# Kernel tuning notes

Hardware: AMD Instinct MI355X
Metric: run time of the kernel (lower is better)

Reference implementation:

```python
import jax, jax.numpy as jnp
import numpy as np

W_IMG = 512
H_IMG = 512
D_MODEL = 192
N_FREQ = 8
LN_EPS = 1e-5


def _fourier_pe(coords_norm):
    # coords_norm: [B,K,2] in [0,1); returns [B,K,4*N_FREQ]
    freqs = 2.0 ** jnp.arange(N_FREQ, dtype=jnp.float32)  # [F]
    two_pi = 2.0 * jnp.pi
    x = coords_norm[..., 0:1] * freqs * two_pi  # [B,K,F]
    y = coords_norm[..., 1:2] * freqs * two_pi
    return jnp.concatenate([jnp.sin(x), jnp.cos(x), jnp.sin(y), jnp.cos(y)], axis=-1)


def _bilinear_sample(feat, gx, gy):
    # feat: [B,C,H,W]; gx,gy: [B,K] normalized coords in [-1,1], align_corners=True
    B, C, H, W = feat.shape
    ix = (gx + 1.0) * 0.5 * (W - 1)
    iy = (gy + 1.0) * 0.5 * (H - 1)
    ix0 = jnp.floor(ix)
    iy0 = jnp.floor(iy)
    wx = ix - ix0  # [B,K]
    wy = iy - iy0
    x0 = jnp.clip(ix0.astype(jnp.int32), 0, W - 1)
    x1 = jnp.clip(ix0.astype(jnp.int32) + 1, 0, W - 1)
    y0 = jnp.clip(iy0.astype(jnp.int32), 0, H - 1)
    y1 = jnp.clip(iy0.astype(jnp.int32) + 1, 0, H - 1)
    b = jnp.arange(B)[:, None]  # [B,1] broadcast against [B,K]
    g = lambda y, x: feat[b, :, y, x]  # [B,K,C]
    out = (g(y0, x0) * ((1 - wx) * (1 - wy))[..., None]
           + g(y0, x1) * (wx * (1 - wy))[..., None]
           + g(y1, x0) * ((1 - wx) * wy)[..., None]
           + g(y1, x1) * (wx * wy)[..., None])
    return out  # [B,K,C]


def setup_inputs() -> dict:
    key = jax.random.key(0)
    ks = jax.random.split(key, 16)
    B, K = 8, 4096
    # pixel coordinates in [0, W_IMG-1] x [0, H_IMG-1]
    u = jax.random.uniform(ks[0], (B, K, 2), dtype=jnp.float32)
    coords = u * jnp.array([W_IMG - 1, H_IMG - 1], dtype=jnp.float32)
    L1 = jax.random.normal(ks[1], (B, D_MODEL, 128, 128), dtype=jnp.float32)
    L2 = jax.random.normal(ks[2], (B, D_MODEL, 64, 64), dtype=jnp.float32)
    L3 = jax.random.normal(ks[3], (B, D_MODEL, 32, 32), dtype=jnp.float32)
    L4 = jax.random.normal(ks[4], (B, D_MODEL, 16, 16), dtype=jnp.float32)
    d_in = D_MODEL * 4 + 4 * N_FREQ  # 800
    Wseed_w = jax.random.normal(ks[5], (D_MODEL, d_in), dtype=jnp.float32) / np.sqrt(d_in)
    Wseed_b = jnp.zeros((D_MODEL,), dtype=jnp.float32)
    ln_g = jnp.ones((D_MODEL,), dtype=jnp.float32)
    ln_b = jnp.zeros((D_MODEL,), dtype=jnp.float32)
    Wpos_w = jax.random.normal(ks[6], (D_MODEL, 4 * N_FREQ), dtype=jnp.float32) / np.sqrt(4 * N_FREQ)
    Wpos_b = jnp.zeros((D_MODEL,), dtype=jnp.float32)
    return {"coords": coords, "L1": L1, "L2": L2, "L3": L3, "L4": L4,
            "Wseed_w": Wseed_w, "Wseed_b": Wseed_b, "ln_g": ln_g, "ln_b": ln_b,
            "Wpos_w": Wpos_w, "Wpos_b": Wpos_b}


def reference(coords, L1, L2, L3, L4, Wseed_w, Wseed_b, ln_g, ln_b, Wpos_w, Wpos_b):
    B, K, _ = coords.shape
    # normalized grid in [-1,1] (x uses W, y uses H), align_corners=True convention
    gx = 2.0 * coords[..., 0] / (W_IMG - 1) - 1.0  # [B,K]
    gy = 2.0 * coords[..., 1] / (H_IMG - 1) - 1.0
    center_grid = jnp.stack([gx, gy], axis=-1).reshape(B, K, 1, 2)
    coords_norm = coords / jnp.array([W_IMG, H_IMG], dtype=jnp.float32)
    pe_q = _fourier_pe(coords_norm)  # [B,K,32]
    f1 = _bilinear_sample(L1, gx, gy)
    f2 = _bilinear_sample(L2, gx, gy)
    f3 = _bilinear_sample(L3, gx, gy)
    f4 = _bilinear_sample(L4, gx, gy)
    x = jnp.concatenate([f1, f2, f3, f4, pe_q], axis=-1)  # [B,K,800]
    seed = x @ Wseed_w.T + Wseed_b
    mu = jnp.mean(seed, axis=-1, keepdims=True)
    var = jnp.mean((seed - mu) ** 2, axis=-1, keepdims=True)
    seed = (seed - mu) / jnp.sqrt(var + LN_EPS) * ln_g + ln_b
    pos = pe_q @ Wpos_w.T + Wpos_b
    return (seed, pos, center_grid)
```

## Files before the change

kernel.cpp:

```cpp
#include <hip/hip_runtime.h>
#include <hip/hip_bf16.h>
#include <stdint.h>

typedef unsigned short u16;
typedef short s16x8 __attribute__((ext_vector_type(8)));
typedef float f32x4 __attribute__((ext_vector_type(4)));
typedef uint32_t u32x4 __attribute__((ext_vector_type(4)));

__device__ __forceinline__ uint32_t pack_bf16(float lo, float hi) {
  float2 f; f.x = lo; f.y = hi;
  __hip_bfloat162 h = __float22bfloat162_rn(f);
  union { __hip_bfloat162 h; uint32_t u; } c; c.h = h;
  return c.u;
}
__device__ __forceinline__ u16 f2bf(float f) {
  union { float f; uint32_t u; } a; a.f = f;
  uint32_t u = a.u;
  return (u16)((u + 0x7fffu + ((u >> 16) & 1u)) >> 16);
}
__device__ __forceinline__ float bf2f(uint32_t hbits) {
  union { uint32_t u; float f; } a; a.u = hbits << 16;
  return a.f;
}

__global__ __launch_bounds__(256) void prep_all(
    const float* __restrict__ L1, const float* __restrict__ L2,
    const float* __restrict__ L3, const float* __restrict__ L4,
    const float* __restrict__ ws_w, const float* __restrict__ wp_w,
    u16* __restrict__ T1, u16* __restrict__ T2,
    u16* __restrict__ T3, u16* __restrict__ T4,
    u16* __restrict__ dWs, u16* __restrict__ dWp) {
  const int bid = blockIdx.x;
  const int t = threadIdx.x;

  if (bid >= 2720) {
    int t0 = (bid - 2720) * 256 + t;
    for (int i = t0; i < 39936; i += 8192) {
      const float* s; u16* d; int off;
      if (i < 38400) { s = ws_w; d = dWs; off = 4 * i; }
      else           { s = wp_w; d = dWp; off = 4 * (i - 38400); }
      f32x4 v = *(const f32x4*)(s + off);
      uint2 o;
      o.x = pack_bf16(v.x, v.y);
      o.y = pack_bf16(v.z, v.w);
      *(uint2*)(d + off) = o;
    }
    return;
  }

  const float* src; u16* dst; int HW, tiles, rel;
  if (bid < 2048)      { src = L1; dst = T1; HW = 16384; tiles = 256; rel = bid; }
  else if (bid < 2560) { src = L2; dst = T2; HW = 4096;  tiles = 64;  rel = bid - 2048; }
  else if (bid < 2688) { src = L3; dst = T3; HW = 1024;  tiles = 16;  rel = bid - 2560; }
  else                 { src = L4; dst = T4; HW = 256;   tiles = 4;   rel = bid - 2688; }
  const int b = rel / tiles, hw0 = (rel % tiles) * 64;

  __shared__ uint32_t tileD[96 * 65];
  const float* sb = src + (size_t)b * 192 * HW + hw0;
  for (int i = 0; i < 6; ++i) {
    int idx = i * 256 + t;
    int c2 = idx >> 4, hw4 = idx & 15;
    f32x4 a = *(const f32x4*)(sb + (size_t)(2 * c2) * HW + hw4 * 4);
    f32x4 c = *(const f32x4*)(sb + (size_t)(2 * c2 + 1) * HW + hw4 * 4);
    uint32_t* w = &tileD[c2 * 65 + hw4 * 4];
    w[0] = pack_bf16(a.x, c.x);
    w[1] = pack_bf16(a.y, c.y);
    w[2] = pack_bf16(a.z, c.z);
    w[3] = pack_bf16(a.w, c.w);
  }
  __syncthreads();
  uint32_t* d = (uint32_t*)(dst + ((size_t)b * HW + hw0) * 192);
  for (int i = 0; i < 12; ++i) {
    int e = i * 256 + t;
    int hw = e / 48, cp = e - hw * 48;
    uint2 v;
    v.x = tileD[(cp * 2) * 65 + hw];
    v.y = tileD[(cp * 2 + 1) * 65 + hw];
    *(uint2*)(d + hw * 96 + cp * 2) = v;
  }
}

__global__ __launch_bounds__(256, 4) void seed_main(
    const float* __restrict__ coords,
    const u16* __restrict__ T1, const u16* __restrict__ T2,
    const u16* __restrict__ T3, const u16* __restrict__ T4,
    const u16* __restrict__ Wseed, const u16* __restrict__ Wpos,
    const float* __restrict__ seed_b, const float* __restrict__ ln_g,
    const float* __restrict__ ln_b, const float* __restrict__ pos_b,
    float* __restrict__ out_seed, float* __restrict__ out_pos,
    float* __restrict__ out_cg) {

  __shared__ __align__(16) u16 xt[16 * 808];
  __shared__ float mu_s[16], rs_s[16];

  const int t = threadIdx.x;
  const int gp0 = blockIdx.x * 16;
  const int b = gp0 >> 12;

  if (t < 32) {
    int p = t >> 1, xy = t & 1;
    float c = coords[(gp0 + p) * 2 + xy];
    out_cg[(gp0 + p) * 2 + xy] = c * (2.0f / 511.0f) - 1.0f;
  }
  for (int i = 0; i < 2; ++i) {
    int e = i * 256 + t;
    int p = e >> 5, j = e & 31;
    float c = coords[(gp0 + p) * 2 + ((j >> 4) & 1)] * (1.0f / 512.0f);
    float v = c * (float)(1 << (j & 7));
    float a = (v - floorf(v)) * 6.283185307179586f;
    float r = (j & 8) ? __cosf(a) : __sinf(a);
    xt[p * 808 + 768 + j] = f2bf(r);
  }

  {
    const u16* B1 = T1 + (size_t)b * 16384 * 192;
    const u16* B2 = T2 + (size_t)b * 4096 * 192;
    const u16* B3 = T3 + (size_t)b * 1024 * 192;
    const u16* B4 = T4 + (size_t)b * 256 * 192;
    int plv = t >> 2;
    int lv = plv & 3, p = plv >> 2;
    int c4b = t & 3;
    float cx = coords[(gp0 + p) * 2 + 0];
    float cy = coords[(gp0 + p) * 2 + 1];
    float gx = cx * (2.0f / 511.0f) - 1.0f;
    float gy = cy * (2.0f / 511.0f) - 1.0f;
    int Wl = 128 >> lv;
    float ix = (gx + 1.0f) * 0.5f * (float)(Wl - 1);
    float iy = (gy + 1.0f) * 0.5f * (float)(Wl - 1);
    float fx = floorf(ix), fy = floorf(iy);
    float wx = ix - fx, wy = iy - fy;
    int x0 = (int)fx, y0 = (int)fy;
    int x1 = min(max(x0 + 1, 0), Wl - 1), y1 = min(max(y0 + 1, 0), Wl - 1);
    x0 = min(max(x0, 0), Wl - 1); y0 = min(max(y0, 0), Wl - 1);
    const u16* base = (lv == 0) ? B1 : (lv == 1) ? B2 : (lv == 2) ? B3 : B4;
    const u16* b00 = base + (y0 * Wl + x0) * 192;
    const u16* b01 = base + (y0 * Wl + x1) * 192;
    const u16* b10 = base + (y1 * Wl + x0) * 192;
    const u16* b11 = base + (y1 * Wl + x1) * 192;
    float w00 = (1.0f - wx) * (1.0f - wy), w01 = wx * (1.0f - wy);
    float w10 = (1.0f - wx) * wy,          w11 = wx * wy;
    u16* dstp = xt + p * 808 + lv * 192;
#pragma unroll
    for (int i = 0; i < 6; ++i) {
      int cc = (c4b + 4 * i) * 8;
      u32x4 q00 = *(const u32x4*)(b00 + cc);
      u32x4 q01 = *(const u32x4*)(b01 + cc);
      u32x4 q10 = *(const u32x4*)(b10 + cc);
      u32x4 q11 = *(const u32x4*)(b11 + cc);
      u32x4 o;
#pragma unroll
      for (int k = 0; k < 4; ++k) {
        float lo = bf2f(q00[k] & 0xffff) * w00 + bf2f(q01[k] & 0xffff) * w01 +
                   bf2f(q10[k] & 0xffff) * w10 + bf2f(q11[k] & 0xffff) * w11;
        float hi = bf2f(q00[k] >> 16) * w00 + bf2f(q01[k] >> 16) * w01 +
                   bf2f(q10[k] >> 16) * w10 + bf2f(q11[k] >> 16) * w11;
        o[k] = pack_bf16(lo, hi);
      }
      *(u32x4*)(dstp + cc) = o;
    }
  }
  __syncthreads();

  const int lid = t & 63, wv = t >> 6;
  const int quad = lid >> 4, mrow = lid & 15;
  const int nt0 = wv * 3;

  f32x4 accS[3], accP[3];
#pragma unroll
  for (int j = 0; j < 3; ++j) { accS[j] = (f32x4)0.0f; accP[j] = (f32x4)0.0f; }

  const u16* wp0 = Wseed + (size_t)((nt0 + 0) * 16 + mrow) * 800 + quad * 8;
  const u16* wp1 = wp0 + 16 * 800;
  const u16* wp2 = wp1 + 16 * 800;
  const u16* arow = xt + mrow * 808 + quad * 8;

  s16x8 a_last;
#pragma unroll 5
  for (int kc = 0; kc < 25; ++kc) {
    int ko = kc * 32;
    s16x8 a = *(const s16x8*)(arow + ko);
    s16x8 b0 = *(const s16x8*)(wp0 + ko);
    s16x8 b1 = *(const s16x8*)(wp1 + ko);
    s16x8 b2 = *(const s16x8*)(wp2 + ko);
    accS[0] = __builtin_amdgcn_mfma_f32_16x16x32_bf16(a, b0, accS[0], 0, 0, 0);
    accS[1] = __builtin_amdgcn_mfma_f32_16x16x32_bf16(a, b1, accS[1], 0, 0, 0);
    accS[2] = __builtin_amdgcn_mfma_f32_16x16x32_bf16(a, b2, accS[2], 0, 0, 0);
    if (kc == 24) a_last = a;
  }
#pragma unroll
  for (int j = 0; j < 3; ++j) {
    int n = (nt0 + j) * 16 + mrow;
    s16x8 bw = *(const s16x8*)(Wpos + n * 32 + quad * 8);
    accP[j] = __builtin_amdgcn_mfma_f32_16x16x32_bf16(a_last, bw, accP[j], 0, 0, 0);
  }

#pragma unroll
  for (int j = 0; j < 3; ++j) {
    int n = (nt0 + j) * 16 + mrow;
    float pb = pos_b[n];
#pragma unroll
    for (int r = 0; r < 4; ++r)
      out_pos[(size_t)(gp0 + quad * 4 + r) * 192 + n] = accP[j][r] + pb;
  }

  __syncthreads();
  float* preLN = (float*)xt;
#pragma unroll
  for (int j = 0; j < 3; ++j) {
    int n = (nt0 + j) * 16 + mrow;
    float sb = seed_b[n];
#pragma unroll
    for (int r = 0; r < 4; ++r)
      preLN[(quad * 4 + r) * 193 + n] = accS[j][r] + sb;
  }
  __syncthreads();

  {
    int r = t >> 4, g = t & 15;
    float s = 0.0f, sq = 0.0f;
#pragma unroll
    for (int i = 0; i < 12; ++i) {
      float v = preLN[r * 193 + g * 12 + i];
      s += v; sq += v * v;
    }
#pragma unroll
    for (int d = 8; d > 0; d >>= 1) {
      s += __shfl_down(s, d, 16);
      sq += __shfl_down(sq, d, 16);
    }
    if (g == 0) {
      float mu = s * (1.0f / 192.0f);
      float var = sq * (1.0f / 192.0f) - mu * mu;
      mu_s[r] = mu;
      rs_s[r] = 1.0f / sqrtf(var + 1e-5f);
    }
  }
  __syncthreads();

  for (int i = 0; i < 12; ++i) {
    int e = i * 256 + t;
    int r = e / 192, n = e - r * 192;
    float v = (preLN[r * 193 + n] - mu_s[r]) * rs_s[r] * ln_g[n] + ln_b[n];
    out_seed[(size_t)(gp0 + r) * 192 + n] = v;
  }
}

extern "C" void kernel_launch(void* const* d_in, const int* in_sizes, int n_in,
                              void* d_out, int out_size, void* d_ws, size_t ws_size,
                              hipStream_t stream) {
  const float* coords  = (const float*)d_in[0];
  const float* L1      = (const float*)d_in[1];
  const float* L2      = (const float*)d_in[2];
  const float* L3      = (const float*)d_in[3];
  const float* L4      = (const float*)d_in[4];
  const float* Wseed_w = (const float*)d_in[5];
  const float* Wseed_b = (const float*)d_in[6];
  const float* ln_g    = (const float*)d_in[7];
  const float* ln_b    = (const float*)d_in[8];
  const float* Wpos_w  = (const float*)d_in[9];
  const float* Wpos_b  = (const float*)d_in[10];

  u16* T1  = (u16*)d_ws;
  u16* T2  = T1 + (size_t)8 * 16384 * 192;
  u16* T3  = T2 + (size_t)8 * 4096 * 192;
  u16* T4  = T3 + (size_t)8 * 1024 * 192;
  u16* Wsd = T4 + (size_t)8 * 256 * 192;
  u16* Wps = Wsd + 153600;

  prep_all<<<2752, 256, 0, stream>>>(L1, L2, L3, L4, Wseed_w, Wpos_w,
                                     T1, T2, T3, T4, Wsd, Wps);

  float* out_seed = (float*)d_out;
  float* out_pos  = out_seed + (size_t)32768 * 192;
  float* out_cg   = out_pos  + (size_t)32768 * 192;

  seed_main<<<2048, 256, 0, stream>>>(coords, T1, T2, T3, T4, Wsd, Wps,
                                      Wseed_b, ln_g, ln_b, Wpos_b,
                                      out_seed, out_pos, out_cg);
}
```

Measured before the change: 273.9 us.

## Process 32 points per block, prefetch GEMM operands, fuse LayerNorm in registers

Result: slower. 279.5 us (+2.0%).

```diff
diff --git a/kernel.cpp b/kernel.cpp
--- a/kernel.cpp
+++ b/kernel.cpp
@@ -80,7 +80,7 @@
   }
 }
 
-__global__ __launch_bounds__(256, 4) void seed_main(
+__global__ __launch_bounds__(256, 3) void seed_main(
     const float* __restrict__ coords,
     const u16* __restrict__ T1, const u16* __restrict__ T2,
     const u16* __restrict__ T3, const u16* __restrict__ T4,
@@ -90,19 +90,19 @@
     float* __restrict__ out_seed, float* __restrict__ out_pos,
     float* __restrict__ out_cg) {
 
-  __shared__ __align__(16) u16 xt[16 * 808];
-  __shared__ float mu_s[16], rs_s[16];
+  __shared__ __align__(16) u16 xt[32 * 808];
+  __shared__ float part_s[32][4], part_q[32][4];
 
   const int t = threadIdx.x;
-  const int gp0 = blockIdx.x * 16;
+  const int gp0 = blockIdx.x * 32;
   const int b = gp0 >> 12;
 
-  if (t < 32) {
+  if (t < 64) {
     int p = t >> 1, xy = t & 1;
     float c = coords[(gp0 + p) * 2 + xy];
     out_cg[(gp0 + p) * 2 + xy] = c * (2.0f / 511.0f) - 1.0f;
   }
-  for (int i = 0; i < 2; ++i) {
+  for (int i = 0; i < 4; ++i) {
     int e = i * 256 + t;
     int p = e >> 5, j = e & 31;
     float c = coords[(gp0 + p) * 2 + ((j >> 4) & 1)] * (1.0f / 512.0f);
@@ -117,9 +117,9 @@
     const u16* B2 = T2 + (size_t)b * 4096 * 192;
     const u16* B3 = T3 + (size_t)b * 1024 * 192;
     const u16* B4 = T4 + (size_t)b * 256 * 192;
-    int plv = t >> 2;
+    int plv = t >> 1;
     int lv = plv & 3, p = plv >> 2;
-    int c4b = t & 3;
+    int half = t & 1;
     float cx = coords[(gp0 + p) * 2 + 0];
     float cy = coords[(gp0 + p) * 2 + 1];
     float gx = cx * (2.0f / 511.0f) - 1.0f;
@@ -133,30 +133,36 @@
     int x1 = min(max(x0 + 1, 0), Wl - 1), y1 = min(max(y0 + 1, 0), Wl - 1);
     x0 = min(max(x0, 0), Wl - 1); y0 = min(max(y0, 0), Wl - 1);
     const u16* base = (lv == 0) ? B1 : (lv == 1) ? B2 : (lv == 2) ? B3 : B4;
-    const u16* b00 = base + (y0 * Wl + x0) * 192;
-    const u16* b01 = base + (y0 * Wl + x1) * 192;
-    const u16* b10 = base + (y1 * Wl + x0) * 192;
-    const u16* b11 = base + (y1 * Wl + x1) * 192;
+    const u16* b00 = base + (y0 * Wl + x0) * 192 + half * 96;
+    const u16* b01 = base + (y0 * Wl + x1) * 192 + half * 96;
+    const u16* b10 = base + (y1 * Wl + x0) * 192 + half * 96;
+    const u16* b11 = base + (y1 * Wl + x1) * 192 + half * 96;
     float w00 = (1.0f - wx) * (1.0f - wy), w01 = wx * (1.0f - wy);
     float w10 = (1.0f - wx) * wy,          w11 = wx * wy;
-    u16* dstp = xt + p * 808 + lv * 192;
-#pragma unroll
-    for (int i = 0; i < 6; ++i) {
-      int cc = (c4b + 4 * i) * 8;
-      u32x4 q00 = *(const u32x4*)(b00 + cc);
-      u32x4 q01 = *(const u32x4*)(b01 + cc);
-      u32x4 q10 = *(const u32x4*)(b10 + cc);
-      u32x4 q11 = *(const u32x4*)(b11 + cc);
-      u32x4 o;
+    u16* dstp = xt + p * 808 + lv * 192 + half * 96;
+#pragma unroll
+    for (int ii = 0; ii < 6; ++ii) {
+      int ca = ii * 16, cb = ii * 16 + 8;
+      u32x4 qa00 = *(const u32x4*)(b00 + ca), qb00 = *(const u32x4*)(b00 + cb);
+      u32x4 qa01 = *(const u32x4*)(b01 + ca), qb01 = *(const u32x4*)(b01 + cb);
+      u32x4 qa10 = *(const u32x4*)(b10 + ca), qb10 = *(const u32x4*)(b10 + cb);
+      u32x4 qa11 = *(const u32x4*)(b11 + ca), qb11 = *(const u32x4*)(b11 + cb);
+      u32x4 oa, ob;
 #pragma unroll
       for (int k = 0; k < 4; ++k) {
-        float lo = bf2f(q00[k] & 0xffff) * w00 + bf2f(q01[k] & 0xffff) * w01 +
-                   bf2f(q10[k] & 0xffff) * w10 + bf2f(q11[k] & 0xffff) * w11;
-        float hi = bf2f(q00[k] >> 16) * w00 + bf2f(q01[k] >> 16) * w01 +
-                   bf2f(q10[k] >> 16) * w10 + bf2f(q11[k] >> 16) * w11;
-        o[k] = pack_bf16(lo, hi);
-      }
-      *(u32x4*)(dstp + cc) = o;
+        float lo = bf2f(qa00[k] & 0xffff) * w00 + bf2f(qa01[k] & 0xffff) * w01 +
+                   bf2f(qa10[k] & 0xffff) * w10 + bf2f(qa11[k] & 0xffff) * w11;
+        float hi = bf2f(qa00[k] >> 16) * w00 + bf2f(qa01[k] >> 16) * w01 +
+                   bf2f(qa10[k] >> 16) * w10 + bf2f(qa11[k] >> 16) * w11;
+        oa[k] = pack_bf16(lo, hi);
+        lo = bf2f(qb00[k] & 0xffff) * w00 + bf2f(qb01[k] & 0xffff) * w01 +
+             bf2f(qb10[k] & 0xffff) * w10 + bf2f(qb11[k] & 0xffff) * w11;
+        hi = bf2f(qb00[k] >> 16) * w00 + bf2f(qb01[k] >> 16) * w01 +
+             bf2f(qb10[k] >> 16) * w10 + bf2f(qb11[k] >> 16) * w11;
+        ob[k] = pack_bf16(lo, hi);
+      }
+      *(u32x4*)(dstp + ca) = oa;
+      *(u32x4*)(dstp + cb) = ob;
     }
   }
   __syncthreads();
@@ -165,83 +171,120 @@
   const int quad = lid >> 4, mrow = lid & 15;
   const int nt0 = wv * 3;
 
-  f32x4 accS[3], accP[3];
-#pragma unroll
-  for (int j = 0; j < 3; ++j) { accS[j] = (f32x4)0.0f; accP[j] = (f32x4)0.0f; }
-
-  const u16* wp0 = Wseed + (size_t)((nt0 + 0) * 16 + mrow) * 800 + quad * 8;
-  const u16* wp1 = wp0 + 16 * 800;
-  const u16* wp2 = wp1 + 16 * 800;
-  const u16* arow = xt + mrow * 808 + quad * 8;
-
-  s16x8 a_last;
-#pragma unroll 5
+  const u16* arow0 = xt + mrow * 808 + quad * 8;
+  const u16* arow1 = arow0 + 16 * 808;
+  const u16* w0 = Wseed + (size_t)((nt0 + 0) * 16 + mrow) * 800 + quad * 8;
+  const u16* w1 = w0 + 16 * 800;
+  const u16* w2 = w1 + 16 * 800;
+
+  f32x4 accS[2][3];
+#pragma unroll
+  for (int mt = 0; mt < 2; ++mt)
+#pragma unroll
+    for (int j = 0; j < 3; ++j) accS[mt][j] = (f32x4)0.0f;
+
+  s16x8 abuf[3][2], bbuf[3][3];
+#pragma unroll
+  for (int s = 0; s < 3; ++s) {
+    int ko = s * 32;
+    abuf[s][0] = *(const s16x8*)(arow0 + ko);
+    abuf[s][1] = *(const s16x8*)(arow1 + ko);
+    bbuf[s][0] = *(const s16x8*)(w0 + ko);
+    bbuf[s][1] = *(const s16x8*)(w1 + ko);
+    bbuf[s][2] = *(const s16x8*)(w2 + ko);
+  }
+#pragma unroll
   for (int kc = 0; kc < 25; ++kc) {
-    int ko = kc * 32;
-    s16x8 a = *(const s16x8*)(arow + ko);
-    s16x8 b0 = *(const s16x8*)(wp0 + ko);
-    s16x8 b1 = *(const s16x8*)(wp1 + ko);
-    s16x8 b2 = *(const s16x8*)(wp2 + ko);
-    accS[0] = __builtin_amdgcn_mfma_f32_16x16x32_bf16(a, b0, accS[0], 0, 0, 0);
-    accS[1] = __builtin_amdgcn_mfma_f32_16x16x32_bf16(a, b1, accS[1], 0, 0, 0);
-    accS[2] = __builtin_amdgcn_mfma_f32_16x16x32_bf16(a, b2, accS[2], 0, 0, 0);
-    if (kc == 24) a_last = a;
-  }
+    const int cur = kc % 3;
+    s16x8 a0 = abuf[cur][0], a1 = abuf[cur][1];
+    s16x8 b0 = bbuf[cur][0], b1 = bbuf[cur][1], b2 = bbuf[cur][2];
+    int nk = kc + 3;
+    if (nk < 25) {
+      int ko = nk * 32;
+      abuf[cur][0] = *(const s16x8*)(arow0 + ko);
+      abuf[cur][1] = *(const s16x8*)(arow1 + ko);
+      bbuf[cur][0] = *(const s16x8*)(w0 + ko);
+      bbuf[cur][1] = *(const s16x8*)(w1 + ko);
+      bbuf[cur][2] = *(const s16x8*)(w2 + ko);
+    }
+    accS[0][0] = __builtin_amdgcn_mfma_f32_16x16x32_bf16(a0, b0, accS[0][0], 0, 0, 0);
+    accS[1][0] = __builtin_amdgcn_mfma_f32_16x16x32_bf16(a1, b0, accS[1][0], 0, 0, 0);
+    accS[0][1] = __builtin_amdgcn_mfma_f32_16x16x32_bf16(a0, b1, accS[0][1], 0, 0, 0);
+    accS[1][1] = __builtin_amdgcn_mfma_f32_16x16x32_bf16(a1, b1, accS[1][1], 0, 0, 0);
+    accS[0][2] = __builtin_amdgcn_mfma_f32_16x16x32_bf16(a0, b2, accS[0][2], 0, 0, 0);
+    accS[1][2] = __builtin_amdgcn_mfma_f32_16x16x32_bf16(a1, b2, accS[1][2], 0, 0, 0);
+  }
+
+  {
+    s16x8 ap0 = *(const s16x8*)(arow0 + 768);
+    s16x8 ap1 = *(const s16x8*)(arow1 + 768);
+#pragma unroll
+    for (int j = 0; j < 3; ++j) {
+      int n = (nt0 + j) * 16 + mrow;
+      s16x8 bw = *(const s16x8*)(Wpos + n * 32 + quad * 8);
+      f32x4 p0 = (f32x4)0.0f, p1 = (f32x4)0.0f;
+      p0 = __builtin_amdgcn_mfma_f32_16x16x32_bf16(ap0, bw, p0, 0, 0, 0);
+      p1 = __builtin_amdgcn_mfma_f32_16x16x32_bf16(ap1, bw, p1, 0, 0, 0);
+      float pb = pos_b[n];
+#pragma unroll
+      for (int r = 0; r < 4; ++r) {
+        out_pos[(size_t)(gp0 + quad * 4 + r) * 192 + n] = p0[r] + pb;
+        out_pos[(size_t)(gp0 + 16 + quad * 4 + r) * 192 + n] = p1[r] + pb;
+      }
+    }
+  }
+
 #pragma unroll
   for (int j = 0; j < 3; ++j) {
-    int n = (nt0 + j) * 16 + mrow;
-    s16x8 bw = *(const s16x8*)(Wpos + n * 32 + quad * 8);
-    accP[j] = __builtin_amdgcn_mfma_f32_16x16x32_bf16(a_last, bw, accP[j], 0, 0, 0);
-  }
-
-#pragma unroll
-  for (int j = 0; j < 3; ++j) {
-    int n = (nt0 + j) * 16 + mrow;
-    float pb = pos_b[n];
-#pragma unroll
-    for (int r = 0; r < 4; ++r)
-      out_pos[(size_t)(gp0 + quad * 4 + r) * 192 + n] = accP[j][r] + pb;
-  }
-
+    float sb = seed_b[(nt0 + j) * 16 + mrow];
+#pragma unroll
+    for (int mt = 0; mt < 2; ++mt)
+#pragma unroll
+      for (int r = 0; r < 4; ++r) accS[mt][j][r] += sb;
+  }
+#pragma unroll
+  for (int mt = 0; mt < 2; ++mt)
+#pragma unroll
+    for (int r = 0; r < 4; ++r) {
+      float s = accS[mt][0][r] + accS[mt][1][r] + accS[mt][2][r];
+      float q = accS[mt][0][r] * accS[mt][0][r] + accS[mt][1][r] * accS[mt][1][r] +
+                accS[mt][2][r] * accS[mt][2][r];
+#pragma unroll
+      for (int d = 1; d < 16; d <<= 1) {
+        s += __shfl_xor(s, d, 16);
+        q += __shfl_xor(q, d, 16);
+      }
+      if (mrow == 0) {
+        int row = mt * 16 + quad * 4 + r;
+        part_s[row][wv] = s;
+        part_q[row][wv] = q;
+      }
+    }
   __syncthreads();
-  float* preLN = (float*)xt;
-#pragma unroll
-  for (int j = 0; j < 3; ++j) {
-    int n = (nt0 + j) * 16 + mrow;
-    float sb = seed_b[n];
-#pragma unroll
-    for (int r = 0; r < 4; ++r)
-      preLN[(quad * 4 + r) * 193 + n] = accS[j][r] + sb;
-  }
-  __syncthreads();
-
-  {
-    int r = t >> 4, g = t & 15;
-    float s = 0.0f, sq = 0.0f;
-#pragma unroll
-    for (int i = 0; i < 12; ++i) {
-      float v = preLN[r * 193 + g * 12 + i];
-      s += v; sq += v * v;
-    }
-#pragma unroll
-    for (int d = 8; d > 0; d >>= 1) {
-      s += __shfl_down(s, d, 16);
-      sq += __shfl_down(sq, d, 16);
-    }
-    if (g == 0) {
-      float mu = s * (1.0f / 192.0f);
-      float var = sq * (1.0f / 192.0f) - mu * mu;
-      mu_s[r] = mu;
-      rs_s[r] = 1.0f / sqrtf(var + 1e-5f);
-    }
-  }
-  __syncthreads();
-
-  for (int i = 0; i < 12; ++i) {
-    int e = i * 256 + t;
-    int r = e / 192, n = e - r * 192;
-    float v = (preLN[r * 193 + n] - mu_s[r]) * rs_s[r] * ln_g[n] + ln_b[n];
-    out_seed[(size_t)(gp0 + r) * 192 + n] = v;
+
+#pragma unroll
+  for (int mt = 0; mt < 2; ++mt) {
+    float mu[4], rs[4];
+#pragma unroll
+    for (int r = 0; r < 4; ++r) {
+      int row = mt * 16 + quad * 4 + r;
+      float s = part_s[row][0] + part_s[row][1] + part_s[row][2] + part_s[row][3];
+      float q = part_q[row][0] + part_q[row][1] + part_q[row][2] + part_q[row][3];
+      float m = s * (1.0f / 192.0f);
+      float var = q * (1.0f / 192.0f) - m * m;
+      mu[r] = m;
+      rs[r] = rsqrtf(var + 1e-5f);
+    }
+#pragma unroll
+    for (int j = 0; j < 3; ++j) {
+      int n = (nt0 + j) * 16 + mrow;
+      float g = ln_g[n], bb = ln_b[n];
+#pragma unroll
+      for (int r = 0; r < 4; ++r) {
+        int row = gp0 + mt * 16 + quad * 4 + r;
+        out_seed[(size_t)row * 192 + n] = (accS[mt][j][r] - mu[r]) * rs[r] * g + bb;
+      }
+    }
   }
 }
 
@@ -274,7 +317,7 @@
   float* out_pos  = out_seed + (size_t)32768 * 192;
   float* out_cg   = out_pos  + (size_t)32768 * 192;
 
-  seed_main<<<2048, 256, 0, stream>>>(coords, T1, T2, T3, T4, Wsd, Wps,
+  seed_main<<<1024, 256, 0, stream>>>(coords, T1, T2, T3, T4, Wsd, Wps,
                                       Wseed_b, ln_g, ln_b, Wpos_b,
                                       out_seed, out_pos, out_cg);
 }
```
